# Kernel optimization log

Hardware: AMD Instinct MI355X
Metric: run time of the kernel (lower is better)

Reference implementation:

```python
import jax, jax.numpy as jnp
import numpy as np

B = 16384            # rays per chunk
NUM_BINS = 129       # num_samples + 1 fenceposts
RESAMPLE_PADDING = 0.01


def setup_inputs() -> dict:
    key = jax.random.key(0)
    k1, k2, k3, k4, k5 = jax.random.split(key, 5)
    origins = jax.random.normal(k1, (B, 3), dtype=jnp.float32)
    d = jax.random.normal(k2, (B, 3), dtype=jnp.float32)
    directions = d / jnp.linalg.norm(d, axis=-1, keepdims=True)
    radii = jax.random.uniform(k3, (B, 1), dtype=jnp.float32, minval=0.001, maxval=0.005)
    # sorted fencepost distances in [near=2, far=6]
    t_vals = jnp.sort(jax.random.uniform(k4, (B, NUM_BINS), dtype=jnp.float32, minval=2.0, maxval=6.0), axis=-1)
    weights = jax.random.uniform(k5, (B, NUM_BINS - 1), dtype=jnp.float32)
    return dict(origins=origins, directions=directions, radii=radii, t_vals=t_vals, weights=weights)


def _piecewise_constant_pdf(bins, weights, num_samples):
    """Inverse-CDF sampling (randomized=False). Math identical to the torch
    mask/max/min formulation: searchsorted(cdf, u, 'right') gives the first
    index with cdf > u (the min over ~mask), and idx-1 the last index with
    cdf <= u (the max over mask); u in [0, 1-eps) so indices are in range."""
    eps = 1e-5
    wsum = jnp.sum(weights, axis=-1, keepdims=True)
    pad = jnp.maximum(0.0, eps - wsum)
    weights = weights + pad / weights.shape[-1]
    wsum = wsum + pad
    pdf = weights / wsum
    cdf = jnp.minimum(1.0, jnp.cumsum(pdf[..., :-1], axis=-1))
    cdf = jnp.concatenate([jnp.zeros_like(cdf[..., :1]), cdf, jnp.ones_like(cdf[..., :1])], axis=-1)  # [B, bins]
    u = jnp.linspace(0.0, 1.0 - jnp.finfo(jnp.float32).eps, num_samples, dtype=jnp.float32)
    u = jnp.broadcast_to(u, cdf.shape[:-1] + (num_samples,))
    idx1 = jax.vmap(lambda c, uu: jnp.searchsorted(c, uu, side='right'))(cdf, u)
    idx1 = jnp.clip(idx1, 1, cdf.shape[-1] - 1)
    idx0 = idx1 - 1
    take = lambda x, i: jnp.take_along_axis(x, i, axis=-1)
    bins_g0, bins_g1 = take(bins, idx0), take(bins, idx1)
    cdf_g0, cdf_g1 = take(cdf, idx0), take(cdf, idx1)
    t = jnp.clip(jnp.nan_to_num((u - cdf_g0) / (cdf_g1 - cdf_g0), nan=0.0), 0.0, 1.0)
    return bins_g0 + t * (bins_g1 - bins_g0)


def _conical_frustum_to_gaussian(d, t0, t1, base_radius):
    """Stable cone->Gaussian (diag covariance), lifted along ray axis d."""
    mu = (t0 + t1) / 2
    hw = (t1 - t0) / 2
    denom = 3 * mu ** 2 + hw ** 2
    t_mean = mu + 2 * mu * hw ** 2 / denom
    t_var = hw ** 2 / 3 - 4 / 15 * (hw ** 4 * (12 * mu ** 2 - hw ** 2) / denom ** 2)
    r_var = base_radius ** 2 * (mu ** 2 / 4 + 5 / 12 * hw ** 2 - 4 / 15 * hw ** 4 / denom)
    mean = d[..., None, :] * t_mean[..., None]                       # [B, S, 3]
    d_mag_sq = jnp.sum(d ** 2, axis=-1, keepdims=True) + 1e-10
    d_outer_diag = d ** 2
    null_outer_diag = 1 - d_outer_diag / d_mag_sq
    cov_diag = t_var[..., None] * d_outer_diag[..., None, :] + r_var[..., None] * null_outer_diag[..., None, :]
    return mean, cov_diag


def reference(origins, directions, radii, t_vals, weights):
    # blur weights (max-pool then avg of neighbors) + padding
    wpad = jnp.concatenate([weights[..., :1], weights, weights[..., -1:]], axis=-1)
    wmax = jnp.maximum(wpad[..., :-1], wpad[..., 1:])
    wblur = 0.5 * (wmax[..., :-1] + wmax[..., 1:])
    w = wblur + RESAMPLE_PADDING
    # stop_grad=True in the torch module (torch.no_grad around resampling)
    new_t_vals = jax.lax.stop_gradient(_piecewise_constant_pdf(t_vals, w, t_vals.shape[-1]))
    t0, t1 = new_t_vals[..., :-1], new_t_vals[..., 1:]
    means, covs = _conical_frustum_to_gaussian(directions, t0, t1, radii)
    means = means + origins[..., None, :]
    return new_t_vals, means, covs
```

## Files before the change

kernel.cpp:

```cpp
#include <hip/hip_runtime.h>

#define NRAYS 16384
#define NB 129
#define NW 128

__global__ __launch_bounds__(256) void mipnerf_waveind_kernel(
    const float* __restrict__ origins,
    const float* __restrict__ directions,
    const float* __restrict__ radii,
    const float* __restrict__ t_vals,
    const float* __restrict__ weights,
    float* __restrict__ out_t,
    float* __restrict__ out_means,
    float* __restrict__ out_covs)
{
    __shared__ __align__(16) float s_nt  [4][NB + 3];
    __shared__ __align__(16) float s_mean[4][NW * 3];
    __shared__ __align__(16) float s_cov [4][NW * 3];

    const int tid = threadIdx.x;
    const int wv  = tid >> 6;
    const int l   = tid & 63;
    const int ray = (blockIdx.x << 2) + wv;

    const float2 wp = *reinterpret_cast<const float2*>(weights + (long)ray * NW + 2 * l);
    const float w0 = wp.x, w1 = wp.y;
    const float* trow = t_vals + (long)ray * NB;
    const float b0 = trow[2 * l];
    const float b1 = trow[2 * l + 1];
    const float b2 = trow[2 * l + 2];

    const float dx = directions[ray * 3 + 0];
    const float dy = directions[ray * 3 + 1];
    const float dz = directions[ray * 3 + 2];
    const float ox = origins[ray * 3 + 0];
    const float oy = origins[ray * 3 + 1];
    const float oz = origins[ray * 3 + 2];
    const float rad = radii[ray];

    float wm1 = __shfl_up(w1, 1);   if (l == 0)  wm1 = w0;
    float wp1 = __shfl_down(w0, 1); if (l == 63) wp1 = w1;
    const float mx01 = fmaxf(w0, w1);
    const float wb0 = 0.5f * (fmaxf(wm1, w0) + mx01) + 0.01f;
    const float wb1 = 0.5f * (mx01 + fmaxf(w1, wp1)) + 0.01f;

    float S = wb0 + wb1;
    #pragma unroll
    for (int off = 1; off < 64; off <<= 1) {
        const float t = __shfl_up(S, off);
        if (l >= off) S += t;
    }
    const float W1 = S;
    const float W0 = S - wb1;
    const float inv_wsum = 1.0f / __shfl(S, 63);

    const float c_lo  = (l == 0)  ? 0.0f : fminf(1.0f, (W0 - wb0) * inv_wsum);
    const float c_mid = fminf(1.0f, W0 * inv_wsum);
    const float c_hi  = (l == 63) ? 1.0f : fminf(1.0f, W1 * inv_wsum);

    const float ueps     = 1.0f - 1.1920929e-7f;
    const float step     = ueps / 128.0f;
    const float inv_step = 128.0f / ueps;
    const int s0 = (int)ceilf(c_lo  * inv_step);
    const int s1 = (int)ceilf(c_mid * inv_step);
    const int s2 = (int)ceilf(c_hi  * inv_step);

    float* ntrow = s_nt[wv];
    {
        const float inv_d = 1.0f / (c_mid - c_lo);
        const float db = b1 - b0;
        for (int s = s0; s < s1; ++s) {
            float tt = ((float)s * step - c_lo) * inv_d;
            tt = fminf(fmaxf(tt, 0.0f), 1.0f);
            ntrow[s] = fmaf(tt, db, b0);
        }
    }
    {
        const float inv_d = 1.0f / (c_hi - c_mid);
        const float db = b2 - b1;
        for (int s = s1; s < s2; ++s) {
            float tt = ((float)s * step - c_mid) * inv_d;
            tt = fminf(fmaxf(tt, 0.0f), 1.0f);
            ntrow[s] = fmaf(tt, db, b1);
        }
    }
    __builtin_amdgcn_wave_barrier();

    const float n0 = ntrow[2 * l];
    const float n1 = ntrow[2 * l + 1];
    const float n2 = ntrow[2 * l + 2];

    const float rad2 = rad * rad;
    const float dx2 = dx * dx, dy2 = dy * dy, dz2 = dz * dz;
    const float inv_dms = 1.0f / (dx2 + dy2 + dz2 + 1e-10f);
    const float nullx = 1.0f - dx2 * inv_dms;
    const float nully = 1.0f - dy2 * inv_dms;
    const float nullz = 1.0f - dz2 * inv_dms;

    float* mrow = s_mean[wv] + 6 * l;
    float* crow = s_cov[wv]  + 6 * l;
    const float tt0[2] = { n0, n1 };
    const float tt1[2] = { n1, n2 };
    #pragma unroll
    for (int k = 0; k < 2; ++k) {
        const float mu = 0.5f * (tt0[k] + tt1[k]);
        const float hw = 0.5f * (tt1[k] - tt0[k]);
        const float mu2 = mu * mu, hw2 = hw * hw;
        const float inv_denom = 1.0f / (3.0f * mu2 + hw2);
        const float t_mean = mu + 2.0f * mu * hw2 * inv_denom;
        const float t_var  = hw2 * (1.0f / 3.0f)
                           - (4.0f / 15.0f) * (hw2 * hw2 * (12.0f * mu2 - hw2) * inv_denom * inv_denom);
        const float r_var  = rad2 * (0.25f * mu2 + (5.0f / 12.0f) * hw2
                                     - (4.0f / 15.0f) * hw2 * hw2 * inv_denom);
        mrow[3 * k + 0] = fmaf(dx, t_mean, ox);
        mrow[3 * k + 1] = fmaf(dy, t_mean, oy);
        mrow[3 * k + 2] = fmaf(dz, t_mean, oz);
        crow[3 * k + 0] = fmaf(t_var, dx2, r_var * nullx);
        crow[3 * k + 1] = fmaf(t_var, dy2, r_var * nully);
        crow[3 * k + 2] = fmaf(t_var, dz2, r_var * nullz);
    }
    __builtin_amdgcn_wave_barrier();

    float* po = out_t + (long)ray * NB;
    po[l]      = ntrow[l];
    po[64 + l] = ntrow[64 + l];
    if (l == 0) po[128] = ntrow[128];

    float4* pm = reinterpret_cast<float4*>(out_means + (long)ray * (NW * 3));
    float4* pc = reinterpret_cast<float4*>(out_covs  + (long)ray * (NW * 3));
    const float4* sm = reinterpret_cast<const float4*>(s_mean[wv]);
    const float4* sc = reinterpret_cast<const float4*>(s_cov[wv]);
    pm[l] = sm[l];
    pc[l] = sc[l];
    if (l < 32) {
        pm[64 + l] = sm[64 + l];
        pc[64 + l] = sc[64 + l];
    }
}

extern "C" void kernel_launch(void* const* d_in, const int* in_sizes, int n_in,
                              void* d_out, int out_size, void* d_ws, size_t ws_size,
                              hipStream_t stream) {
    const float* origins    = (const float*)d_in[0];
    const float* directions = (const float*)d_in[1];
    const float* radii      = (const float*)d_in[2];
    const float* t_vals     = (const float*)d_in[3];
    const float* weights    = (const float*)d_in[4];

    float* out_t     = (float*)d_out;
    float* out_means = out_t + (long)NRAYS * NB;
    float* out_covs  = out_means + (long)NRAYS * NW * 3;

    const int grid = NRAYS / 4;
    mipnerf_waveind_kernel<<<grid, 256, 0, stream>>>(
        origins, directions, radii, t_vals, weights, out_t, out_means, out_covs);
}
```

Measured before the change: 19.28 us.

## Process two rays per wavefront with four bins per lane and direct stores

```diff
diff --git a/kernel.cpp b/kernel.cpp
--- a/kernel.cpp
+++ b/kernel.cpp
@@ -4,7 +4,7 @@
 #define NB 129
 #define NW 128
 
-__global__ __launch_bounds__(256) void mipnerf_waveind_kernel(
+__global__ __launch_bounds__(256) void mipnerf_2ray_kernel(
     const float* __restrict__ origins,
     const float* __restrict__ directions,
     const float* __restrict__ radii,
@@ -14,21 +14,23 @@
     float* __restrict__ out_means,
     float* __restrict__ out_covs)
 {
-    __shared__ __align__(16) float s_nt  [4][NB + 3];
-    __shared__ __align__(16) float s_mean[4][NW * 3];
-    __shared__ __align__(16) float s_cov [4][NW * 3];
+    __shared__ __align__(16) float s_nt[4][2][132];
 
-    const int tid = threadIdx.x;
-    const int wv  = tid >> 6;
-    const int l   = tid & 63;
-    const int ray = (blockIdx.x << 2) + wv;
+    const int tid  = threadIdx.x;
+    const int wv   = tid >> 6;
+    const int l    = tid & 63;
+    const int half = l >> 5;
+    const int l5   = l & 31;
+    const int w    = (blockIdx.x << 2) + wv;
+    const int ray  = (w << 1) + half;
 
-    const float2 wp = *reinterpret_cast<const float2*>(weights + (long)ray * NW + 2 * l);
-    const float w0 = wp.x, w1 = wp.y;
+    const float4 wf = *reinterpret_cast<const float4*>(weights + (long)ray * NW + 4 * l5);
+    const float w0 = wf.x, w1 = wf.y, w2 = wf.z, w3 = wf.w;
+
     const float* trow = t_vals + (long)ray * NB;
-    const float b0 = trow[2 * l];
-    const float b1 = trow[2 * l + 1];
-    const float b2 = trow[2 * l + 2];
+    float b[5];
+    #pragma unroll
+    for (int j = 0; j < 5; ++j) b[j] = trow[4 * l5 + j];
 
     const float dx = directions[ray * 3 + 0];
     const float dy = directions[ray * 3 + 1];
@@ -38,57 +40,56 @@
     const float oz = origins[ray * 3 + 2];
     const float rad = radii[ray];
 
-    float wm1 = __shfl_up(w1, 1);   if (l == 0)  wm1 = w0;
-    float wp1 = __shfl_down(w0, 1); if (l == 63) wp1 = w1;
-    const float mx01 = fmaxf(w0, w1);
-    const float wb0 = 0.5f * (fmaxf(wm1, w0) + mx01) + 0.01f;
-    const float wb1 = 0.5f * (mx01 + fmaxf(w1, wp1)) + 0.01f;
+    float wm1 = __shfl_up(w3, 1);   if (l5 == 0)  wm1 = w0;
+    float wp1 = __shfl_down(w0, 1); if (l5 == 31) wp1 = w3;
+    float wb[4];
+    wb[0] = 0.5f * (fmaxf(wm1, w0) + fmaxf(w0, w1)) + 0.01f;
+    wb[1] = 0.5f * (fmaxf(w0, w1) + fmaxf(w1, w2)) + 0.01f;
+    wb[2] = 0.5f * (fmaxf(w1, w2) + fmaxf(w2, w3)) + 0.01f;
+    wb[3] = 0.5f * (fmaxf(w2, w3) + fmaxf(w3, wp1)) + 0.01f;
 
-    float S = wb0 + wb1;
+    float S = (wb[0] + wb[1]) + (wb[2] + wb[3]);
     #pragma unroll
-    for (int off = 1; off < 64; off <<= 1) {
+    for (int off = 1; off < 32; off <<= 1) {
         const float t = __shfl_up(S, off);
-        if (l >= off) S += t;
+        if (l5 >= off) S += t;
     }
-    const float W1 = S;
-    const float W0 = S - wb1;
-    const float inv_wsum = 1.0f / __shfl(S, 63);
+    const float inv_wsum = 1.0f / __shfl(S, (l & 32) | 31);
 
-    const float c_lo  = (l == 0)  ? 0.0f : fminf(1.0f, (W0 - wb0) * inv_wsum);
-    const float c_mid = fminf(1.0f, W0 * inv_wsum);
-    const float c_hi  = (l == 63) ? 1.0f : fminf(1.0f, W1 * inv_wsum);
+    const float P4 = S;
+    const float P3 = P4 - wb[3];
+    const float P2 = P3 - wb[2];
+    const float P1 = P2 - wb[1];
+    const float P0 = P1 - wb[0];
+    float c[5];
+    c[0] = (l5 == 0)  ? 0.0f : fminf(1.0f, P0 * inv_wsum);
+    c[1] = fminf(1.0f, P1 * inv_wsum);
+    c[2] = fminf(1.0f, P2 * inv_wsum);
+    c[3] = fminf(1.0f, P3 * inv_wsum);
+    c[4] = (l5 == 31) ? 1.0f : fminf(1.0f, P4 * inv_wsum);
 
     const float ueps     = 1.0f - 1.1920929e-7f;
     const float step     = ueps / 128.0f;
     const float inv_step = 128.0f / ueps;
-    const int s0 = (int)ceilf(c_lo  * inv_step);
-    const int s1 = (int)ceilf(c_mid * inv_step);
-    const int s2 = (int)ceilf(c_hi  * inv_step);
+    int sidx[5];
+    #pragma unroll
+    for (int j = 0; j < 5; ++j) sidx[j] = (int)ceilf(c[j] * inv_step);
 
-    float* ntrow = s_nt[wv];
-    {
-        const float inv_d = 1.0f / (c_mid - c_lo);
-        const float db = b1 - b0;
-        for (int s = s0; s < s1; ++s) {
-            float tt = ((float)s * step - c_lo) * inv_d;
+    float* ntrow = s_nt[wv][half];
+    #pragma unroll
+    for (int j = 0; j < 4; ++j) {
+        const float inv_d = 1.0f / (c[j + 1] - c[j]);
+        const float db = b[j + 1] - b[j];
+        for (int s = sidx[j]; s < sidx[j + 1]; ++s) {
+            float tt = ((float)s * step - c[j]) * inv_d;
             tt = fminf(fmaxf(tt, 0.0f), 1.0f);
-            ntrow[s] = fmaf(tt, db, b0);
-        }
-    }
-    {
-        const float inv_d = 1.0f / (c_hi - c_mid);
-        const float db = b2 - b1;
-        for (int s = s1; s < s2; ++s) {
-            float tt = ((float)s * step - c_mid) * inv_d;
-            tt = fminf(fmaxf(tt, 0.0f), 1.0f);
-            ntrow[s] = fmaf(tt, db, b1);
+            ntrow[s] = fmaf(tt, db, b[j]);
         }
     }
     __builtin_amdgcn_wave_barrier();
 
-    const float n0 = ntrow[2 * l];
-    const float n1 = ntrow[2 * l + 1];
-    const float n2 = ntrow[2 * l + 2];
+    const float4 n4 = *reinterpret_cast<const float4*>(ntrow + 4 * l5);
+    const float nt[5] = { n4.x, n4.y, n4.z, n4.w, ntrow[4 * l5 + 4] };
 
     const float rad2 = rad * rad;
     const float dx2 = dx * dx, dy2 = dy * dy, dz2 = dz * dz;
@@ -97,14 +98,11 @@
     const float nully = 1.0f - dy2 * inv_dms;
     const float nullz = 1.0f - dz2 * inv_dms;
 
-    float* mrow = s_mean[wv] + 6 * l;
-    float* crow = s_cov[wv]  + 6 * l;
-    const float tt0[2] = { n0, n1 };
-    const float tt1[2] = { n1, n2 };
+    float m[12], cv[12];
     #pragma unroll
-    for (int k = 0; k < 2; ++k) {
-        const float mu = 0.5f * (tt0[k] + tt1[k]);
-        const float hw = 0.5f * (tt1[k] - tt0[k]);
+    for (int k = 0; k < 4; ++k) {
+        const float mu = 0.5f * (nt[k] + nt[k + 1]);
+        const float hw = 0.5f * (nt[k + 1] - nt[k]);
         const float mu2 = mu * mu, hw2 = hw * hw;
         const float inv_denom = 1.0f / (3.0f * mu2 + hw2);
         const float t_mean = mu + 2.0f * mu * hw2 * inv_denom;
@@ -112,30 +110,27 @@
                            - (4.0f / 15.0f) * (hw2 * hw2 * (12.0f * mu2 - hw2) * inv_denom * inv_denom);
         const float r_var  = rad2 * (0.25f * mu2 + (5.0f / 12.0f) * hw2
                                      - (4.0f / 15.0f) * hw2 * hw2 * inv_denom);
-        mrow[3 * k + 0] = fmaf(dx, t_mean, ox);
-        mrow[3 * k + 1] = fmaf(dy, t_mean, oy);
-        mrow[3 * k + 2] = fmaf(dz, t_mean, oz);
-        crow[3 * k + 0] = fmaf(t_var, dx2, r_var * nullx);
-        crow[3 * k + 1] = fmaf(t_var, dy2, r_var * nully);
-        crow[3 * k + 2] = fmaf(t_var, dz2, r_var * nullz);
+        m[3 * k + 0]  = fmaf(dx, t_mean, ox);
+        m[3 * k + 1]  = fmaf(dy, t_mean, oy);
+        m[3 * k + 2]  = fmaf(dz, t_mean, oz);
+        cv[3 * k + 0] = fmaf(t_var, dx2, r_var * nullx);
+        cv[3 * k + 1] = fmaf(t_var, dy2, r_var * nully);
+        cv[3 * k + 2] = fmaf(t_var, dz2, r_var * nullz);
     }
-    __builtin_amdgcn_wave_barrier();
+
+    float4* pm = reinterpret_cast<float4*>(out_means + (long)ray * (NW * 3)) + 3 * l5;
+    float4* pc = reinterpret_cast<float4*>(out_covs  + (long)ray * (NW * 3)) + 3 * l5;
+    pm[0] = make_float4(m[0], m[1], m[2],  m[3]);
+    pm[1] = make_float4(m[4], m[5], m[6],  m[7]);
+    pm[2] = make_float4(m[8], m[9], m[10], m[11]);
+    pc[0] = make_float4(cv[0], cv[1], cv[2],  cv[3]);
+    pc[1] = make_float4(cv[4], cv[5], cv[6],  cv[7]);
+    pc[2] = make_float4(cv[8], cv[9], cv[10], cv[11]);
 
     float* po = out_t + (long)ray * NB;
-    po[l]      = ntrow[l];
-    po[64 + l] = ntrow[64 + l];
-    if (l == 0) po[128] = ntrow[128];
-
-    float4* pm = reinterpret_cast<float4*>(out_means + (long)ray * (NW * 3));
-    float4* pc = reinterpret_cast<float4*>(out_covs  + (long)ray * (NW * 3));
-    const float4* sm = reinterpret_cast<const float4*>(s_mean[wv]);
-    const float4* sc = reinterpret_cast<const float4*>(s_cov[wv]);
-    pm[l] = sm[l];
-    pc[l] = sc[l];
-    if (l < 32) {
-        pm[64 + l] = sm[64 + l];
-        pc[64 + l] = sc[64 + l];
-    }
+    #pragma unroll
+    for (int k = 0; k < 4; ++k) po[l5 + 32 * k] = ntrow[l5 + 32 * k];
+    if (l5 == 0) po[128] = ntrow[128];
 }
 
 extern "C" void kernel_launch(void* const* d_in, const int* in_sizes, int n_in,
@@ -151,7 +146,7 @@
     float* out_means = out_t + (long)NRAYS * NB;
     float* out_covs  = out_means + (long)NRAYS * NW * 3;
 
-    const int grid = NRAYS / 4;
-    mipnerf_waveind_kernel<<<grid, 256, 0, stream>>>(
+    const int grid = NRAYS / 8;
+    mipnerf_2ray_kernel<<<grid, 256, 0, stream>>>(
         origins, directions, radii, t_vals, weights, out_t, out_means, out_covs);
 }
```

After: 22.81 us. 1.18x slower.
